# Optimization experiments

Measured on AMD Instinct MI355X. Metric: run time of the kernel, lower is better.

## Reference

```python
import jax, jax.numpy as jnp
import numpy as np

D_MODEL = 1024
N_HEADS = 16
D_FF = 4 * D_MODEL
CTX = 2048
EPS = 1e-5


def setup_inputs() -> dict:
    key = jax.random.key(0)
    ks = jax.random.split(key, 8)
    s = 0.02
    z = jax.random.normal(ks[0], (2, CTX, D_MODEL), dtype=jnp.float32)
    W_Q = jax.random.normal(ks[1], (D_MODEL, D_MODEL), dtype=jnp.float32) * s
    W_K = jax.random.normal(ks[2], (D_MODEL, D_MODEL), dtype=jnp.float32) * s
    W_V = jax.random.normal(ks[3], (D_MODEL, D_MODEL), dtype=jnp.float32) * s
    W_O = jax.random.normal(ks[4], (D_MODEL, D_MODEL), dtype=jnp.float32) * s
    W_fc = jax.random.normal(ks[5], (D_MODEL, D_FF), dtype=jnp.float32) * s
    W_proj = jax.random.normal(ks[6], (D_FF, D_MODEL), dtype=jnp.float32) * s
    g1 = jnp.ones((D_MODEL,), dtype=jnp.float32)
    g2 = jnp.ones((D_MODEL,), dtype=jnp.float32)
    return {"z": z, "W_Q": W_Q, "W_K": W_K, "W_V": W_V, "W_O": W_O,
            "W_fc": W_fc, "W_proj": W_proj, "g1": g1, "g2": g2}


def rmsnorm(x, gain):
    rms = jnp.sqrt(jnp.sum(x * x, axis=-1, keepdims=True) / x.shape[-1] + EPS)
    return (x / rms) * gain


def gelu_erf(x):
    return x * 0.5 * (1.0 + jax.lax.erf(x / jnp.sqrt(2.0).astype(x.dtype)))


def attention(zn, W_Q, W_K, W_V, W_O):
    B, T, D = zn.shape
    H = N_HEADS
    dh = D // H
    # [B,T,D] -> [B,H,T,dh]
    def split(x):
        return x.reshape(B, T, H, dh).transpose(0, 2, 1, 3)
    Q = split(zn @ W_Q)
    K = split(zn @ W_K)
    V = split(zn @ W_V)
    scores = jnp.einsum('bhtd,bhsd->bhts', Q, K) / jnp.sqrt(jnp.float32(dh))
    causal = jnp.triu(jnp.ones((T, T), dtype=bool), k=1)  # True above diagonal -> masked
    scores = jnp.where(causal[None, None], -jnp.inf, scores)
    weights = jax.nn.softmax(scores, axis=-1)
    ctx = jnp.einsum('bhts,bhsd->bhtd', weights, V)
    ctx = ctx.transpose(0, 2, 1, 3).reshape(B, T, D)
    return ctx @ W_O


def reference(z, W_Q, W_K, W_V, W_O, W_fc, W_proj, g1, g2):
    # pre-norm GPT block: z + attn(norm1(z)); then + ffn(norm2(z))
    z = z + attention(rmsnorm(z, g1), W_Q, W_K, W_V, W_O)
    h = rmsnorm(z, g2)
    ffn = gelu_erf(h @ W_fc) @ W_proj
    return z + ffn
```

## Files before the change

### kernel.cpp

```cpp
#include <hip/hip_runtime.h>
#include <hip/hip_bf16.h>
#include <math.h>


typedef __bf16 bf16x8 __attribute__((ext_vector_type(8)));
typedef float  f32x4  __attribute__((ext_vector_type(4)));

#define MFMA_16x16x32_BF16(A, B, C) __builtin_amdgcn_mfma_f32_16x16x32_bf16((A), (B), (C), 0, 0, 0)

#define GLDS16(g, l) __builtin_amdgcn_global_load_lds( \
    (const __attribute__((address_space(1))) void*)(g), \
    (__attribute__((address_space(3))) void*)(l), 16, 0, 0)

__device__ __forceinline__ float fmax3(float a, float b, float c) {
    return fmaxf(fmaxf(a, b), c);
}

__global__ __launch_bounds__(256) void fused_head_kernel(
    const float* __restrict__ W_Q, const float* __restrict__ W_K,
    const float* __restrict__ W_V, const float* __restrict__ W_O,
    const float* __restrict__ W_fc, const float* __restrict__ W_proj,
    __bf16* __restrict__ WtQKV, __bf16* __restrict__ WtO,
    __bf16* __restrict__ Wtfc, __bf16* __restrict__ Wtproj,
    const float* __restrict__ z, const float* __restrict__ g1,
    __bf16* __restrict__ zn)
{
    const int id = blockIdx.x;
    if (id >= 12288) {
        const int row = id - 12288, t = threadIdx.x;
        const float4 v = ((const float4*)(z + (size_t)row * 1024))[t];
        float ss = v.x * v.x + v.y * v.y + v.z * v.z + v.w * v.w;
#pragma unroll
        for (int m = 1; m < 64; m <<= 1) ss += __shfl_xor(ss, m);
        __shared__ float red[4];
        const int wid = t >> 6, lane = t & 63;
        if (lane == 0) red[wid] = ss;
        __syncthreads();
        const float tot = red[0] + red[1] + red[2] + red[3];
        const float inv = rsqrtf(tot * (1.0f / 1024.0f) + 1e-5f);
        const float4 gv = ((const float4*)g1)[t];
        __bf16* o = zn + (size_t)row * 1024 + t * 4;
        o[0] = (__bf16)(v.x * inv * gv.x);
        o[1] = (__bf16)(v.y * inv * gv.y);
        o[2] = (__bf16)(v.z * inv * gv.z);
        o[3] = (__bf16)(v.w * inv * gv.w);
        return;
    }
    const float* src;
    __bf16* dst;
    int K, N, nx, t;
    if (id < 4096) {
        const int wsel = id >> 10;
        t = id & 1023;
        src = (wsel == 0) ? W_Q : (wsel == 1) ? W_K : (wsel == 2) ? W_V : W_O;
        dst = (wsel < 3) ? (WtQKV + (size_t)wsel * 1048576) : WtO;
        K = 1024; N = 1024; nx = 32;
    } else if (id < 8192) {
        t = id - 4096; src = W_fc; dst = Wtfc; K = 1024; N = 4096; nx = 128;
    } else {
        t = id - 8192; src = W_proj; dst = Wtproj; K = 4096; N = 1024; nx = 32;
    }
    const int n0 = (t % nx) * 32, k0 = (t / nx) * 32;

    __shared__ float tile[32][33];
    const int c = threadIdx.x & 31, r = threadIdx.x >> 5;
#pragma unroll
    for (int i = 0; i < 4; ++i)
        tile[r + 8 * i][c] = src[(size_t)(k0 + r + 8 * i) * N + n0 + c];
    __syncthreads();
#pragma unroll
    for (int i = 0; i < 4; ++i)
        dst[(size_t)(n0 + r + 8 * i) * K + k0 + c] = (__bf16)tile[c][r + 8 * i];
}

__global__ __launch_bounds__(256) void rmsnorm_kernel(
    const float* __restrict__ x, const float* __restrict__ gain,
    __bf16* __restrict__ out)
{
    const int row = blockIdx.x, t = threadIdx.x;
    const float4 v = ((const float4*)(x + (size_t)row * 1024))[t];
    float ss = v.x * v.x + v.y * v.y + v.z * v.z + v.w * v.w;
#pragma unroll
    for (int m = 1; m < 64; m <<= 1) ss += __shfl_xor(ss, m);
    __shared__ float red[4];
    const int wid = t >> 6, lane = t & 63;
    if (lane == 0) red[wid] = ss;
    __syncthreads();
    const float tot = red[0] + red[1] + red[2] + red[3];
    const float inv = rsqrtf(tot * (1.0f / 1024.0f) + 1e-5f);
    const float4 gv = ((const float4*)gain)[t];
    __bf16* o = out + (size_t)row * 1024 + t * 4;
    o[0] = (__bf16)(v.x * inv * gv.x);
    o[1] = (__bf16)(v.y * inv * gv.y);
    o[2] = (__bf16)(v.z * inv * gv.z);
    o[3] = (__bf16)(v.w * inv * gv.w);
}

__global__ __launch_bounds__(256) void reduce_add_kernel(
    float* __restrict__ out, const __bf16* __restrict__ p0,
    const __bf16* __restrict__ p1, int n8)
{
    for (int i = blockIdx.x * 256 + threadIdx.x; i < n8; i += gridDim.x * 256) {
        const bf16x8 a = ((const bf16x8*)p0)[i];
        const bf16x8 b = ((const bf16x8*)p1)[i];
        float4 o0 = ((float4*)out)[2 * i];
        float4 o1 = ((float4*)out)[2 * i + 1];
        o0.x += (float)a[0] + (float)b[0]; o0.y += (float)a[1] + (float)b[1];
        o0.z += (float)a[2] + (float)b[2]; o0.w += (float)a[3] + (float)b[3];
        o1.x += (float)a[4] + (float)b[4]; o1.y += (float)a[5] + (float)b[5];
        o1.z += (float)a[6] + (float)b[6]; o1.w += (float)a[7] + (float)b[7];
        ((float4*)out)[2 * i] = o0;
        ((float4*)out)[2 * i + 1] = o1;
    }
}

template <int EPI>
__device__ __forceinline__ void epi_write(
    void* outp, const float* res, int N, int rowg, int colg, float v)
{
    if constexpr (EPI == 1) {
        const size_t idx = (size_t)rowg * N + colg;
        ((float*)outp)[idx] = res[idx] + v;
    } else if constexpr (EPI == 2) {
        const size_t idx = (size_t)rowg * N + colg;
        const float u = v * (1.0f + 0.044715f * v * v) * 2.3022585093f;
        const float r = __builtin_amdgcn_rcpf(1.0f + exp2f(u));
        ((__bf16*)outp)[idx] = (__bf16)(v - v * r);
    }
}

template <int EPI>
__global__ __launch_bounds__(512, 2) void gemm256(
    const __bf16* __restrict__ A, const __bf16* __restrict__ Bt,
    void* __restrict__ outp, const float* __restrict__ res,
    int M, int N, int K)
{
    __shared__ __bf16 As[2][2][128 * 64];
    __shared__ __bf16 Bs[2][2][128 * 64];
    const int tid = threadIdx.x;

    const int gx = gridDim.x, nwg = gx * gridDim.y;
    int bid = blockIdx.y * gx + blockIdx.x;
    int m0, n0;
    if (gx == 16 && gridDim.y == 16) {
        const int xcd = bid & 7, c = bid >> 3;
        const int rm = xcd >> 1, rn = xcd & 1;
        m0 = (rm * 4 + (c >> 3)) * 256;
        n0 = (rn * 8 + (c & 7)) * 256;
    } else {
        if ((nwg & 7) == 0) bid = (bid & 7) * (nwg >> 3) + (bid >> 3);
        m0 = (bid / gx) * 256; n0 = (bid % gx) * 256;
    }

    const int lane = tid & 63, w = tid >> 6;
    const int wr = w >> 2, wc = w & 3;
    const int lr = lane & 15, g = lane >> 4;
    const int srow8 = lane >> 3, schunk = (lane & 7) ^ srow8;
    const int xk = lr & 7;
    const int wch = wc >> 1, bro = (wc & 1) * 64;

    const __bf16* Ab = A + (size_t)m0 * K;
    const __bf16* Bb = Bt + (size_t)n0 * K;

    auto STG = [&](const __bf16* gb, __bf16* lds, int kt, int half) {
        const __bf16* src = gb + (size_t)(half * 128) * K + (kt << 6);
#pragma unroll
        for (int j = 0; j < 2; ++j) {
            const int sidx = j * 8 + w;
            GLDS16(src + (size_t)(sidx * 8 + srow8) * K + schunk * 8, lds + sidx * 512);
        }
    };

    f32x4 acc[8][4] = {};
    bf16x8 af[2][4], bf[2][4];

#define LAF(BUF, QM) do {                                                       \
    _Pragma("unroll") for (int i_ = 0; i_ < 4; ++i_)                            \
    _Pragma("unroll") for (int kk_ = 0; kk_ < 2; ++kk_)                         \
        af[kk_][i_] = *(const bf16x8*)&As[BUF][wr]                              \
            [((QM) * 64 + i_ * 16 + lr) * 64 + (((kk_ * 4 + g) ^ xk) << 3)];    \
    } while (0)

#define LBF(BUF, QN) do {                                                       \
    _Pragma("unroll") for (int i_ = 0; i_ < 2; ++i_)                            \
    _Pragma("unroll") for (int kk_ = 0; kk_ < 2; ++kk_)                         \
        bf[kk_][(QN) * 2 + i_] = *(const bf16x8*)&Bs[BUF][wch]                  \
            [(bro + ((QN) * 2 + i_) * 16 + lr) * 64 + (((kk_ * 4 + g) ^ xk) << 3)]; \
    } while (0)

#define MMQ(QM, QN) do {                                                        \
    __builtin_amdgcn_s_setprio(1);                                              \
    _Pragma("unroll") for (int kk_ = 0; kk_ < 2; ++kk_)                         \
    _Pragma("unroll") for (int i_ = 0; i_ < 4; ++i_)                            \
    _Pragma("unroll") for (int n_ = 0; n_ < 2; ++n_)                            \
        acc[(QM) * 4 + i_][(QN) * 2 + n_] = MFMA_16x16x32_BF16(                 \
            af[kk_][i_], bf[kk_][(QN) * 2 + n_], acc[(QM) * 4 + i_][(QN) * 2 + n_]); \
    __builtin_amdgcn_s_setprio(0);                                              \
    } while (0)

#define BAR()  __builtin_amdgcn_s_barrier()
#define VMC(N_) asm volatile("s_waitcnt vmcnt(" #N_ ")" ::: "memory")
#define SGB0() __builtin_amdgcn_sched_barrier(0)

    const int nt = K >> 6, niter = nt >> 1;

    STG(Ab, &As[0][0][0], 0, 0); STG(Ab, &As[0][1][0], 0, 1);
    STG(Bb, &Bs[0][0][0], 0, 0); STG(Bb, &Bs[0][1][0], 0, 1);
    STG(Bb, &Bs[1][0][0], 1, 0); STG(Bb, &Bs[1][1][0], 1, 1);

    for (int i = 0; i < niter - 1; ++i) {
        const int t1 = 2 * i + 1;
        STG(Ab, &As[1][0][0], t1, 0);
        VMC(6); BAR(); SGB0();
        LAF(0, 0); LBF(0, 0); MMQ(0, 0); BAR();
        LBF(0, 1); STG(Ab, &As[1][1][0], t1, 1); BAR(); MMQ(0, 1); BAR();
        LAF(0, 1); STG(Bb, &Bs[0][0][0], t1 + 1, 0); BAR(); MMQ(1, 0); BAR();
        STG(Bb, &Bs[0][1][0], t1 + 1, 1); BAR(); MMQ(1, 1); BAR();
        STG(Ab, &As[0][0][0], t1 + 1, 0);
        VMC(6); BAR(); SGB0();
        LAF(1, 0); LBF(1, 0); MMQ(0, 0); BAR();
        LBF(1, 1); STG(Ab, &As[0][1][0], t1 + 1, 1); BAR(); MMQ(0, 1); BAR();
        LAF(1, 1); STG(Bb, &Bs[1][0][0], t1 + 2, 0); BAR(); MMQ(1, 0); BAR();
        STG(Bb, &Bs[1][1][0], t1 + 2, 1); BAR(); MMQ(1, 1); BAR();
    }
    {
        STG(Ab, &As[1][0][0], nt - 1, 0);
        VMC(6); BAR(); SGB0();
        LAF(0, 0); LBF(0, 0); MMQ(0, 0); BAR();
        LBF(0, 1); STG(Ab, &As[1][1][0], nt - 1, 1); BAR(); MMQ(0, 1); BAR();
        LAF(0, 1); BAR(); MMQ(1, 0); BAR();
        BAR(); MMQ(1, 1); BAR();
        VMC(0); BAR(); SGB0();
        LAF(1, 0); LBF(1, 0); MMQ(0, 0); BAR();
        LBF(1, 1); BAR(); MMQ(0, 1); BAR();
        LAF(1, 1); BAR(); MMQ(1, 0); BAR();
        BAR(); MMQ(1, 1); BAR();
    }
#undef LAF
#undef LBF
#undef MMQ
#undef BAR
#undef VMC
#undef SGB0

#pragma unroll
    for (int mi = 0; mi < 8; ++mi)
#pragma unroll
        for (int ni = 0; ni < 4; ++ni) {
            const int colg = n0 + wc * 64 + ni * 16 + lr;
#pragma unroll
            for (int r = 0; r < 4; ++r) {
                const int rowg = m0 + wr * 128 + mi * 16 + 4 * g + r;
                epi_write<EPI>(outp, res, N, rowg, colg, acc[mi][ni][r]);
            }
        }
}

template <int BM, int BN, int EPI>
__global__ __launch_bounds__(256) void gemm_bf16(
    const __bf16* __restrict__ A, const __bf16* __restrict__ Bt,
    void* __restrict__ outp, const float* __restrict__ res,
    int M, int N, int K, int Kld)
{
    __shared__ __bf16 As[2][BM * 64];
    __shared__ __bf16 Bs[2][BN * 64];
    const int tid = threadIdx.x;

    const int gx = gridDim.x, nwg = gx * gridDim.y;
    int bid = blockIdx.y * gx + blockIdx.x;
    int m0, n0;
    if constexpr (EPI == 4) {
        const int xcd = bid & 7, c = bid >> 3;
        const int rm = xcd >> 1, rn = xcd & 1;
        m0 = (rm * 8 + (c >> 4)) * BM;
        n0 = (rn * 16 + (c & 15)) * BN;
    } else {
        if ((nwg & 7) == 0) bid = (bid & 7) * (nwg >> 3) + (bid >> 3);
        m0 = (bid / gx) * BM; n0 = (bid % gx) * BN;
    }

    const int lane = tid & 63, w = tid >> 6;
    const int wm = w >> 1, wn = w & 1;
    const int lr = lane & 15, g = lane >> 4;
    const int srow = lane >> 3;
    const int scol = ((lane & 7) ^ srow) * 8;
    const int xr8 = lr & 7;

    constexpr int MI = BM / 32, NI = BN / 32;
    f32x4 acc[MI][NI] = {};

    const __bf16* Abase = A + (size_t)m0 * Kld + blockIdx.z * K;
    const __bf16* Bbase = Bt + (size_t)n0 * Kld + blockIdx.z * K;

    auto STAGE = [&](int kb, int buf) {
#pragma unroll
        for (int j = 0; j < BM / 32; ++j) {
            const int s = j * 4 + w;
            GLDS16(Abase + (size_t)(s * 8 + srow) * Kld + kb + scol, &As[buf][s * 512]);
        }
#pragma unroll
        for (int j = 0; j < BN / 32; ++j) {
            const int s = j * 4 + w;
            GLDS16(Bbase + (size_t)(s * 8 + srow) * Kld + kb + scol, &Bs[buf][s * 512]);
        }
    };

    const int nt = K >> 6;
    STAGE(0, 0);
    __syncthreads();

    for (int t = 0; t < nt; ++t) {
        const int cur = t & 1;
        if (t + 1 < nt) STAGE((t + 1) << 6, cur ^ 1);

        bf16x8 af[2][MI], bfr[2][NI];
#pragma unroll
        for (int kk = 0; kk < 2; ++kk) {
#pragma unroll
            for (int i = 0; i < MI; ++i)
                af[kk][i] = *(const bf16x8*)
                    &As[cur][(wm * (BM / 2) + i * 16 + lr) * 64 + (((kk * 4 + g) ^ xr8) << 3)];
#pragma unroll
            for (int i = 0; i < NI; ++i)
                bfr[kk][i] = *(const bf16x8*)
                    &Bs[cur][(wn * (BN / 2) + i * 16 + lr) * 64 + (((kk * 4 + g) ^ xr8) << 3)];
        }
#pragma unroll
        for (int kk = 0; kk < 2; ++kk)
#pragma unroll
            for (int mi = 0; mi < MI; ++mi)
#pragma unroll
                for (int ni = 0; ni < NI; ++ni)
                    acc[mi][ni] = MFMA_16x16x32_BF16(af[kk][mi], bfr[kk][ni], acc[mi][ni]);
        if (t + 1 < nt) __syncthreads();
    }

    if constexpr (EPI == 4) {
        __bf16* vtile = (__bf16*)As;
        const bool hasV = (n0 + BN > 2048);
        if (hasV) __syncthreads();
#pragma unroll
        for (int mi = 0; mi < MI; ++mi)
#pragma unroll
            for (int ni = 0; ni < NI; ++ni) {
                const int colg = n0 + wn * (BN / 2) + ni * 16 + lr;
#pragma unroll
                for (int r = 0; r < 4; ++r) {
                    const int rowg = m0 + wm * (BM / 2) + mi * 16 + 4 * g + r;
                    const float v = acc[mi][ni][r];
                    if (colg < 2048) {
                        ((__bf16*)outp)[(size_t)(colg >> 10) * 4194304 +
                                        (size_t)rowg * 1024 + (colg & 1023)] = (__bf16)v;
                    } else {
                        const int trow = rowg - m0;
                        const int r32 = trow & 31;
                        const int p = ((r32 & 12) << 1) | ((r32 >> 2) & 4) | (r32 & 3);
                        vtile[(colg - n0) * 128 + (trow & ~31) + p] = (__bf16)v;
                    }
                }
            }
        if (hasV) {
            __syncthreads();
            const int vstart = (2048 > n0) ? (2048 - n0) : 0;
            const int nvec = (BN - vstart) * 16;
            __bf16* base = (__bf16*)outp;
            const size_t vt0 = 8388608 + (size_t)((m0 >> 11) * 16) * 64 * 2048 +
                               (m0 & 2047);
            for (int v = tid; v < nvec; v += 256) {
                const int vc = vstart + (v >> 4);
                const int t8 = (v & 15) << 3;
                const int cg = (n0 + vc) & 1023;
                const size_t idx = vt0 + ((size_t)(cg >> 6) * 64 + (cg & 63)) * 2048 + t8;
                *(bf16x8*)&base[idx] = *(const bf16x8*)&vtile[vc * 128 + t8];
            }
        }
    } else {
#pragma unroll
        for (int mi = 0; mi < MI; ++mi)
#pragma unroll
            for (int ni = 0; ni < NI; ++ni) {
                const int colg = n0 + wn * (BN / 2) + ni * 16 + lr;
#pragma unroll
                for (int r = 0; r < 4; ++r) {
                    const int rowg = m0 + wm * (BM / 2) + mi * 16 + 4 * g + r;
                    const float v = acc[mi][ni][r];
                    if constexpr (EPI == 5) {
                        __bf16* pout = (blockIdx.z == 0) ? (__bf16*)outp
                                                         : (__bf16*)(void*)res;
                        pout[(size_t)rowg * N + colg] = (__bf16)v;
                    } else {
                        epi_write<EPI>(outp, res, N, rowg, colg, v);
                    }
                }
            }
    }
}

__global__ __launch_bounds__(512) void attn_kernel(
    const __bf16* __restrict__ Q, const __bf16* __restrict__ Kb,
    const __bf16* __restrict__ Vt, __bf16* __restrict__ ctx)
{
    const int Dm = 1024, T = 2048;
    const int tid = threadIdx.x;
    const int w = tid >> 6, lane = tid & 63;
    const int lr = lane & 15, g = lane >> 4;
    const int bx = blockIdx.x;
    const int j = bx >> 5, bh = bx & 31, b = bh >> 4, h = bh & 15;
    const int qc = (j < 8) ? j : 23 - j;
    const int qbase = qc * 128 + w * 16;
    const size_t rowoff = (size_t)b * T;
    const __bf16* Qp = Q + rowoff * Dm + h * 64;
    const __bf16* Kp = Kb + rowoff * Dm + h * 64;
    const __bf16* Vtp = Vt + (size_t)bh * 64 * 2048;

    __shared__ __bf16 Ks[2][128 * 64];
    __shared__ __bf16 Vs[2][64 * 128];

    bf16x8 qf0 = *(const bf16x8*)&Qp[(size_t)(qbase + lr) * Dm + g * 8];
    bf16x8 qf1 = *(const bf16x8*)&Qp[(size_t)(qbase + lr) * Dm + 32 + g * 8];
    const float qsc = 0.125f * 1.44269504088896340736f;
#pragma unroll
    for (int jj = 0; jj < 8; ++jj) {
        qf0[jj] = (__bf16)((float)qf0[jj] * qsc);
        qf1[jj] = (__bf16)((float)qf1[jj] * qsc);
    }
    bf16x8 ones;
#pragma unroll
    for (int jj = 0; jj < 8; ++jj) ones[jj] = (__bf16)1.0f;

    const int ksrow = lane >> 3;
    const int kschunk = (lane & 7) ^ ksrow;
    const int vsrow = lane >> 4;

    f32x4 acc[4] = {};
    f32x4 accS = {};
    float m_s = -__builtin_inff();
    const int nsteps = qc + 1;
    const f32x4 zacc = {0.0f, 0.0f, 0.0f, 0.0f};
    const int x8 = lr & 7;
    const int qg = qbase + lr;

    auto STAGE = [&](int kvb, int buf) {
#pragma unroll
        for (int jj = 0; jj < 2; ++jj) {
            const int krow = w * 16 + jj * 8;
            GLDS16(Kp + (size_t)(kvb + krow + ksrow) * Dm + kschunk * 8,
                   &Ks[buf][krow * 64]);
            const int vrow = w * 8 + jj * 4;
            const int vchunk = (lane & 15) ^ ((vrow + vsrow) & 15);
            GLDS16(Vtp + (size_t)(vrow + vsrow) * T + kvb + vchunk * 8,
                   &Vs[buf][vrow * 128]);
        }
    };

    STAGE(0, 0);
    __syncthreads();

    for (int t = 0; t < nsteps; ++t) {
        const int kvb = t * 128, cur = t & 1;
        if (t + 1 < nsteps) STAGE(kvb + 128, cur ^ 1);

        float sv[8][4];
        if (t < qc) {
#pragma unroll
            for (int s4 = 0; s4 < 8; ++s4) {
                const int row = s4 * 16 + lr;
                const bf16x8 kfa = *(const bf16x8*)&Ks[cur][row * 64 + ((g ^ x8) << 3)];
                const bf16x8 kfb = *(const bf16x8*)&Ks[cur][row * 64 + (((4 + g) ^ x8) << 3)];
                f32x4 st = MFMA_16x16x32_BF16(kfa, qf0, zacc);
                st = MFMA_16x16x32_BF16(kfb, qf1, st);
#pragma unroll
                for (int r = 0; r < 4; ++r) sv[s4][r] = st[r];
            }
        } else {
#pragma unroll
            for (int s4 = 0; s4 < 8; ++s4) {
                const int kv0 = kvb + s4 * 16;
                if (kv0 <= qbase + 15) {
                    const int row = s4 * 16 + lr;
                    const bf16x8 kfa = *(const bf16x8*)&Ks[cur][row * 64 + ((g ^ x8) << 3)];
                    const bf16x8 kfb = *(const bf16x8*)&Ks[cur][row * 64 + (((4 + g) ^ x8) << 3)];
                    f32x4 st = MFMA_16x16x32_BF16(kfa, qf0, zacc);
                    st = MFMA_16x16x32_BF16(kfb, qf1, st);
                    const bool domask = (kv0 + 15 > qbase);
#pragma unroll
                    for (int r = 0; r < 4; ++r) {
                        float x = st[r];
                        if (domask && (kv0 + 4 * g + r > qg)) x = -__builtin_inff();
                        sv[s4][r] = x;
                    }
                } else {
#pragma unroll
                    for (int r = 0; r < 4; ++r) sv[s4][r] = -__builtin_inff();
                }
            }
        }

        float tml = fmax3(sv[0][0], sv[0][1], sv[0][2]);
        tml = fmax3(tml, sv[0][3], sv[1][0]);
        tml = fmax3(tml, sv[1][1], sv[1][2]);
        tml = fmax3(tml, sv[1][3], sv[2][0]);
        tml = fmax3(tml, sv[2][1], sv[2][2]);
        tml = fmax3(tml, sv[2][3], sv[3][0]);
        tml = fmax3(tml, sv[3][1], sv[3][2]);
        tml = fmax3(tml, sv[3][3], sv[4][0]);
        tml = fmax3(tml, sv[4][1], sv[4][2]);
        tml = fmax3(tml, sv[4][3], sv[5][0]);
        tml = fmax3(tml, sv[5][1], sv[5][2]);
        tml = fmax3(tml, sv[5][3], sv[6][0]);
        tml = fmax3(tml, sv[6][1], sv[6][2]);
        tml = fmax3(tml, sv[6][3], sv[7][0]);
        tml = fmax3(tml, sv[7][1], sv[7][2]);
        tml = fmaxf(tml, sv[7][3]);

        if (!__all(tml - m_s <= 11.5f)) {
            float tm = fmaxf(tml, __shfl_xor(tml, 16));
            tm = fmaxf(tm, __shfl_xor(tm, 32));
            const float m_new = fmaxf(m_s, tm);
            const float corr = exp2f(m_s - m_new);
            float cr[4];
#pragma unroll
            for (int r = 0; r < 4; ++r) cr[r] = __shfl(corr, 4 * g + r);
#pragma unroll
            for (int ct = 0; ct < 4; ++ct) {
                acc[ct][0] *= cr[0]; acc[ct][1] *= cr[1];
                acc[ct][2] *= cr[2]; acc[ct][3] *= cr[3];
            }
            accS[0] *= cr[0]; accS[1] *= cr[1];
            accS[2] *= cr[2]; accS[3] *= cr[3];
            m_s = m_new;
        }

#pragma unroll
        for (int s4 = 0; s4 < 8; ++s4)
#pragma unroll
            for (int r = 0; r < 4; ++r)
                sv[s4][r] = exp2f(sv[s4][r] - m_s);

        bf16x8 pa[4];
#pragma unroll
        for (int s = 0; s < 4; ++s)
#pragma unroll
            for (int r = 0; r < 4; ++r) {
                pa[s][r] = (__bf16)sv[2 * s][r];
                pa[s][4 + r] = (__bf16)sv[2 * s + 1][r];
            }
        if (t < qc) {
#pragma unroll
            for (int s = 0; s < 4; ++s)
                accS = MFMA_16x16x32_BF16(pa[s], ones, accS);
#pragma unroll
            for (int ct = 0; ct < 4; ++ct) {
                const __bf16* vrow = &Vs[cur][(ct * 16 + lr) * 128];
#pragma unroll
                for (int s = 0; s < 4; ++s) {
                    const bf16x8 vf = *(const bf16x8*)&vrow[(((s * 4 + g) ^ lr) << 3)];
                    acc[ct] = MFMA_16x16x32_BF16(pa[s], vf, acc[ct]);
                }
            }
        } else {
#pragma unroll
            for (int s = 0; s < 4; ++s)
                if (kvb + s * 32 <= qbase + 15)
                    accS = MFMA_16x16x32_BF16(pa[s], ones, accS);
#pragma unroll
            for (int ct = 0; ct < 4; ++ct) {
                const __bf16* vrow = &Vs[cur][(ct * 16 + lr) * 128];
#pragma unroll
                for (int s = 0; s < 4; ++s) {
                    if (kvb + s * 32 <= qbase + 15) {
                        const bf16x8 vf = *(const bf16x8*)&vrow[(((s * 4 + g) ^ lr) << 3)];
                        acc[ct] = MFMA_16x16x32_BF16(pa[s], vf, acc[ct]);
                    }
                }
            }
        }
        __syncthreads();
    }

    float dn[4];
#pragma unroll
    for (int r = 0; r < 4; ++r) dn[r] = __builtin_amdgcn_rcpf(accS[r]);
#pragma unroll
    for (int ct = 0; ct < 4; ++ct)
#pragma unroll
        for (int r = 0; r < 4; ++r)
            ctx[(rowoff + qbase + 4 * g + r) * Dm + h * 64 + ct * 16 + lr] =
                (__bf16)(acc[ct][r] * dn[r]);
}

extern "C" void kernel_launch(void* const* d_in, const int* in_sizes, int n_in,
                              void* d_out, int out_size, void* d_ws, size_t ws_size,
                              hipStream_t stream)
{
    (void)in_sizes; (void)n_in; (void)out_size; (void)ws_size;
    const float* z      = (const float*)d_in[0];
    const float* W_Q    = (const float*)d_in[1];
    const float* W_K    = (const float*)d_in[2];
    const float* W_V    = (const float*)d_in[3];
    const float* W_O    = (const float*)d_in[4];
    const float* W_fc   = (const float*)d_in[5];
    const float* W_proj = (const float*)d_in[6];
    const float* g1     = (const float*)d_in[7];
    const float* g2     = (const float*)d_in[8];
    float* out = (float*)d_out;

    char* ws = (char*)d_ws;
    const size_t MB = (size_t)1 << 20;
    __bf16* WtQKV  = (__bf16*)(ws + 0 * MB);
    __bf16* WtO    = (__bf16*)(ws + 6 * MB);
    __bf16* Wtfc   = (__bf16*)(ws + 8 * MB);
    __bf16* Wtproj = (__bf16*)(ws + 16 * MB);
    __bf16* zn     = (__bf16*)(ws + 24 * MB);
    __bf16* Qb     = (__bf16*)(ws + 32 * MB);
    __bf16* Kbuf   = (__bf16*)(ws + 40 * MB);
    __bf16* Vtb    = (__bf16*)(ws + 48 * MB);
    __bf16* ffn1   = (__bf16*)(ws + 40 * MB);
    __bf16* part0  = (__bf16*)(ws + 0 * MB);
    __bf16* part1  = (__bf16*)(ws + 24 * MB);
    __bf16* ctx    = zn;
    __bf16* hb     = Qb;

    const int Tt = 2048, Dm = 1024, Bb = 2, M = Bb * Tt, DFF = 4096;
    const dim3 blk256(256), blk512(512);

    fused_head_kernel<<<16384, blk256, 0, stream>>>(
        W_Q, W_K, W_V, W_O, W_fc, W_proj, WtQKV, WtO, Wtfc, Wtproj, z, g1, zn);

    gemm_bf16<128, 96, 4><<<dim3(32, 32), blk256, 0, stream>>>(
        zn, WtQKV, Qb, nullptr, M, 3072, Dm, Dm);

    attn_kernel<<<512, blk512, 0, stream>>>(Qb, Kbuf, Vtb, ctx);

    gemm_bf16<128, 64, 1><<<dim3(16, 32), blk256, 0, stream>>>(
        ctx, WtO, out, z, M, Dm, Dm, Dm);

    rmsnorm_kernel<<<M, blk256, 0, stream>>>(out, g2, hb);

    gemm256<2><<<dim3(16, 16), blk512, 0, stream>>>(
        hb, Wtfc, ffn1, nullptr, M, DFF, Dm);

    gemm_bf16<128, 128, 5><<<dim3(8, 32, 2), blk256, 0, stream>>>(
        ffn1, Wtproj, part0, (const float*)part1, M, Dm, DFF / 2, DFF);

    reduce_add_kernel<<<2048, blk256, 0, stream>>>(out, part0, part1, M * Dm / 8);
}
```

Measured before the change: 223.2 us.

## Run FFN down-projection with 256x256 tiles and 4-way split-K

Result: slower. 227.7 us (+2.0%).

```diff
diff --git a/kernel.cpp b/kernel.cpp
--- a/kernel.cpp
+++ b/kernel.cpp
@@ -96,19 +96,26 @@
     o[3] = (__bf16)(v.w * inv * gv.w);
 }
 
-__global__ __launch_bounds__(256) void reduce_add_kernel(
+__global__ __launch_bounds__(256) void reduce_add4_kernel(
     float* __restrict__ out, const __bf16* __restrict__ p0,
-    const __bf16* __restrict__ p1, int n8)
+    const __bf16* __restrict__ p1, const __bf16* __restrict__ p2,
+    const __bf16* __restrict__ p3, int n8)
 {
     for (int i = blockIdx.x * 256 + threadIdx.x; i < n8; i += gridDim.x * 256) {
         const bf16x8 a = ((const bf16x8*)p0)[i];
         const bf16x8 b = ((const bf16x8*)p1)[i];
+        const bf16x8 c = ((const bf16x8*)p2)[i];
+        const bf16x8 d = ((const bf16x8*)p3)[i];
         float4 o0 = ((float4*)out)[2 * i];
         float4 o1 = ((float4*)out)[2 * i + 1];
-        o0.x += (float)a[0] + (float)b[0]; o0.y += (float)a[1] + (float)b[1];
-        o0.z += (float)a[2] + (float)b[2]; o0.w += (float)a[3] + (float)b[3];
-        o1.x += (float)a[4] + (float)b[4]; o1.y += (float)a[5] + (float)b[5];
-        o1.z += (float)a[6] + (float)b[6]; o1.w += (float)a[7] + (float)b[7];
+        o0.x += (float)a[0] + (float)b[0] + (float)c[0] + (float)d[0];
+        o0.y += (float)a[1] + (float)b[1] + (float)c[1] + (float)d[1];
+        o0.z += (float)a[2] + (float)b[2] + (float)c[2] + (float)d[2];
+        o0.w += (float)a[3] + (float)b[3] + (float)c[3] + (float)d[3];
+        o1.x += (float)a[4] + (float)b[4] + (float)c[4] + (float)d[4];
+        o1.y += (float)a[5] + (float)b[5] + (float)c[5] + (float)d[5];
+        o1.z += (float)a[6] + (float)b[6] + (float)c[6] + (float)d[6];
+        o1.w += (float)a[7] + (float)b[7] + (float)c[7] + (float)d[7];
         ((float4*)out)[2 * i] = o0;
         ((float4*)out)[2 * i + 1] = o1;
     }
@@ -129,11 +136,13 @@
     }
 }
 
+__device__ __constant__ size_t POFF[4] = {0, 4194304, 12582912, 16777216};
+
 template <int EPI>
 __global__ __launch_bounds__(512, 2) void gemm256(
     const __bf16* __restrict__ A, const __bf16* __restrict__ Bt,
     void* __restrict__ outp, const float* __restrict__ res,
-    int M, int N, int K)
+    int M, int N, int K, int Kld)
 {
     __shared__ __bf16 As[2][2][128 * 64];
     __shared__ __bf16 Bs[2][2][128 * 64];
@@ -159,15 +168,15 @@
     const int xk = lr & 7;
     const int wch = wc >> 1, bro = (wc & 1) * 64;
 
-    const __bf16* Ab = A + (size_t)m0 * K;
-    const __bf16* Bb = Bt + (size_t)n0 * K;
+    const __bf16* Ab = A + (size_t)m0 * Kld + (size_t)blockIdx.z * K;
+    const __bf16* Bb = Bt + (size_t)n0 * Kld + (size_t)blockIdx.z * K;
 
     auto STG = [&](const __bf16* gb, __bf16* lds, int kt, int half) {
-        const __bf16* src = gb + (size_t)(half * 128) * K + (kt << 6);
+        const __bf16* src = gb + (size_t)(half * 128) * Kld + (kt << 6);
 #pragma unroll
         for (int j = 0; j < 2; ++j) {
             const int sidx = j * 8 + w;
-            GLDS16(src + (size_t)(sidx * 8 + srow8) * K + schunk * 8, lds + sidx * 512);
+            GLDS16(src + (size_t)(sidx * 8 + srow8) * Kld + schunk * 8, lds + sidx * 512);
         }
     };
 
@@ -243,17 +252,32 @@
 #undef VMC
 #undef SGB0
 
-#pragma unroll
-    for (int mi = 0; mi < 8; ++mi)
-#pragma unroll
-        for (int ni = 0; ni < 4; ++ni) {
-            const int colg = n0 + wc * 64 + ni * 16 + lr;
-#pragma unroll
-            for (int r = 0; r < 4; ++r) {
-                const int rowg = m0 + wr * 128 + mi * 16 + 4 * g + r;
-                epi_write<EPI>(outp, res, N, rowg, colg, acc[mi][ni][r]);
-            }
-        }
+    if constexpr (EPI == 5) {
+        __bf16* pout = (__bf16*)outp + POFF[blockIdx.z];
+#pragma unroll
+        for (int mi = 0; mi < 8; ++mi)
+#pragma unroll
+            for (int ni = 0; ni < 4; ++ni) {
+                const int colg = n0 + wc * 64 + ni * 16 + lr;
+#pragma unroll
+                for (int r = 0; r < 4; ++r) {
+                    const int rowg = m0 + wr * 128 + mi * 16 + 4 * g + r;
+                    pout[(size_t)rowg * N + colg] = (__bf16)acc[mi][ni][r];
+                }
+            }
+    } else {
+#pragma unroll
+        for (int mi = 0; mi < 8; ++mi)
+#pragma unroll
+            for (int ni = 0; ni < 4; ++ni) {
+                const int colg = n0 + wc * 64 + ni * 16 + lr;
+#pragma unroll
+                for (int r = 0; r < 4; ++r) {
+                    const int rowg = m0 + wr * 128 + mi * 16 + 4 * g + r;
+                    epi_write<EPI>(outp, res, N, rowg, colg, acc[mi][ni][r]);
+                }
+            }
+    }
 }
 
 template <int BM, int BN, int EPI>
@@ -383,14 +407,7 @@
 #pragma unroll
                 for (int r = 0; r < 4; ++r) {
                     const int rowg = m0 + wm * (BM / 2) + mi * 16 + 4 * g + r;
-                    const float v = acc[mi][ni][r];
-                    if constexpr (EPI == 5) {
-                        __bf16* pout = (blockIdx.z == 0) ? (__bf16*)outp
-                                                         : (__bf16*)(void*)res;
-                        pout[(size_t)rowg * N + colg] = (__bf16)v;
-                    } else {
-                        epi_write<EPI>(outp, res, N, rowg, colg, v);
-                    }
+                    epi_write<EPI>(outp, res, N, rowg, colg, acc[mi][ni][r]);
                 }
             }
     }
@@ -617,7 +634,9 @@
     __bf16* Vtb    = (__bf16*)(ws + 48 * MB);
     __bf16* ffn1   = (__bf16*)(ws + 40 * MB);
     __bf16* part0  = (__bf16*)(ws + 0 * MB);
-    __bf16* part1  = (__bf16*)(ws + 24 * MB);
+    __bf16* part1  = (__bf16*)(ws + 8 * MB);
+    __bf16* part2  = (__bf16*)(ws + 24 * MB);
+    __bf16* part3  = (__bf16*)(ws + 32 * MB);
     __bf16* ctx    = zn;
     __bf16* hb     = Qb;
 
@@ -638,10 +657,11 @@
     rmsnorm_kernel<<<M, blk256, 0, stream>>>(out, g2, hb);
 
     gemm256<2><<<dim3(16, 16), blk512, 0, stream>>>(
-        hb, Wtfc, ffn1, nullptr, M, DFF, Dm);
-
-    gemm_bf16<128, 128, 5><<<dim3(8, 32, 2), blk256, 0, stream>>>(
-        ffn1, Wtproj, part0, (const float*)part1, M, Dm, DFF / 2, DFF);
-
-    reduce_add_kernel<<<2048, blk256, 0, stream>>>(out, part0, part1, M * Dm / 8);
-}
+        hb, Wtfc, ffn1, nullptr, M, DFF, Dm, Dm);
+
+    gemm256<5><<<dim3(4, 16, 4), blk512, 0, stream>>>(
+        ffn1, Wtproj, part0, nullptr, M, Dm, DFF / 4, DFF);
+
+    reduce_add4_kernel<<<2048, blk256, 0, stream>>>(
+        out, part0, part1, part2, part3, M * Dm / 8);
+}
```

## Split causal attention KV range in two and add a combine kernel

Applied to the files above, without the earlier changes.

Result: slower. 232.8 us (+4.3%).

```diff
diff --git a/kernel.cpp b/kernel.cpp
--- a/kernel.cpp
+++ b/kernel.cpp
@@ -398,15 +398,17 @@
 
 __global__ __launch_bounds__(512) void attn_kernel(
     const __bf16* __restrict__ Q, const __bf16* __restrict__ Kb,
-    const __bf16* __restrict__ Vt, __bf16* __restrict__ ctx)
+    const __bf16* __restrict__ Vt, __bf16* __restrict__ Op,
+    float* __restrict__ Sp, float* __restrict__ Mp)
 {
     const int Dm = 1024, T = 2048;
     const int tid = threadIdx.x;
     const int w = tid >> 6, lane = tid & 63;
     const int lr = lane & 15, g = lane >> 4;
     const int bx = blockIdx.x;
-    const int j = bx >> 5, bh = bx & 31, b = bh >> 4, h = bh & 15;
-    const int qc = (j < 8) ? j : 23 - j;
+    const int half = bx & 1, up = bx >> 1;
+    const int j = up >> 5, bh = up & 31, b = bh >> 4, h = bh & 15;
+    const int qc = 15 - j;
     const int qbase = qc * 128 + w * 16;
     const size_t rowoff = (size_t)b * T;
     const __bf16* Qp = Q + rowoff * Dm + h * 64;
@@ -434,8 +436,10 @@
 
     f32x4 acc[4] = {};
     f32x4 accS = {};
-    float m_s = -__builtin_inff();
-    const int nsteps = qc + 1;
+    float m_s = 0.0f;
+    const int h0 = (qc + 2) >> 1;
+    const int t0 = half ? h0 : 0;
+    const int t1 = half ? (qc + 1) : h0;
     const f32x4 zacc = {0.0f, 0.0f, 0.0f, 0.0f};
     const int x8 = lr & 7;
     const int qg = qbase + lr;
@@ -453,12 +457,14 @@
         }
     };
 
-    STAGE(0, 0);
-    __syncthreads();
-
-    for (int t = 0; t < nsteps; ++t) {
+    if (t0 < t1) {
+        STAGE(t0 * 128, t0 & 1);
+        __syncthreads();
+    }
+
+    for (int t = t0; t < t1; ++t) {
         const int kvb = t * 128, cur = t & 1;
-        if (t + 1 < nsteps) STAGE(kvb + 128, cur ^ 1);
+        if (t + 1 < t1) STAGE(kvb + 128, cur ^ 1);
 
         float sv[8][4];
         if (t < qc) {
@@ -578,15 +584,51 @@
         __syncthreads();
     }
 
-    float dn[4];
-#pragma unroll
-    for (int r = 0; r < 4; ++r) dn[r] = __builtin_amdgcn_rcpf(accS[r]);
+    const int hb = ((bh * 16 + qc) << 1) | half;
+    __bf16* Oh = Op + (size_t)hb * 8192;
 #pragma unroll
     for (int ct = 0; ct < 4; ++ct)
 #pragma unroll
         for (int r = 0; r < 4; ++r)
-            ctx[(rowoff + qbase + 4 * g + r) * Dm + h * 64 + ct * 16 + lr] =
-                (__bf16)(acc[ct][r] * dn[r]);
+            Oh[(w * 16 + 4 * g + r) * 64 + ct * 16 + lr] = (__bf16)acc[ct][r];
+    if (lr == 0) {
+#pragma unroll
+        for (int r = 0; r < 4; ++r)
+            Sp[hb * 128 + w * 16 + 4 * g + r] = accS[r];
+    }
+    if (g == 0) {
+        Mp[hb * 128 + w * 16 + lr] = m_s;
+    }
+}
+
+__global__ __launch_bounds__(256) void attn_combine_kernel(
+    const __bf16* __restrict__ Op, const float* __restrict__ Sp,
+    const float* __restrict__ Mp, __bf16* __restrict__ ctx)
+{
+    const int u = blockIdx.x;
+    const int bh = u >> 4, qc = u & 15;
+    const int b = bh >> 4, h = bh & 15;
+    const int row = threadIdx.x >> 1, dh = (threadIdx.x & 1) * 32;
+    const int hb0 = u * 2, hb1 = hb0 + 1;
+    const float mA = Mp[hb0 * 128 + row], mB = Mp[hb1 * 128 + row];
+    const float M = fmaxf(mA, mB);
+    const float eA = exp2f(mA - M), eB = exp2f(mB - M);
+    const float den = Sp[hb0 * 128 + row] * eA + Sp[hb1 * 128 + row] * eB;
+    const float inv = __builtin_amdgcn_rcpf(den);
+    const float fA = eA * inv, fB = eB * inv;
+    const __bf16* OA = Op + (size_t)hb0 * 8192 + row * 64 + dh;
+    const __bf16* OB = Op + (size_t)hb1 * 8192 + row * 64 + dh;
+    __bf16* co = ctx + ((size_t)(b * 2048 + qc * 128 + row)) * 1024 + h * 64 + dh;
+#pragma unroll
+    for (int k = 0; k < 4; ++k) {
+        const bf16x8 a = *(const bf16x8*)&OA[k * 8];
+        const bf16x8 bv = *(const bf16x8*)&OB[k * 8];
+        bf16x8 o;
+#pragma unroll
+        for (int e = 0; e < 8; ++e)
+            o[e] = (__bf16)((float)a[e] * fA + (float)bv[e] * fB);
+        *(bf16x8*)&co[k * 8] = o;
+    }
 }
 
 extern "C" void kernel_launch(void* const* d_in, const int* in_sizes, int n_in,
@@ -615,6 +657,9 @@
     __bf16* Qb     = (__bf16*)(ws + 32 * MB);
     __bf16* Kbuf   = (__bf16*)(ws + 40 * MB);
     __bf16* Vtb    = (__bf16*)(ws + 48 * MB);
+    __bf16* Opart  = (__bf16*)(ws + 56 * MB);
+    float*  Spart  = (float*)(ws + 0 * MB);
+    float*  Mpart  = (float*)(ws + 0 * MB + 524288);
     __bf16* ffn1   = (__bf16*)(ws + 40 * MB);
     __bf16* part0  = (__bf16*)(ws + 0 * MB);
     __bf16* part1  = (__bf16*)(ws + 24 * MB);
@@ -630,7 +675,8 @@
     gemm_bf16<128, 96, 4><<<dim3(32, 32), blk256, 0, stream>>>(
         zn, WtQKV, Qb, nullptr, M, 3072, Dm, Dm);
 
-    attn_kernel<<<512, blk512, 0, stream>>>(Qb, Kbuf, Vtb, ctx);
+    attn_kernel<<<1024, blk512, 0, stream>>>(Qb, Kbuf, Vtb, Opart, Spart, Mpart);
+    attn_combine_kernel<<<512, blk256, 0, stream>>>(Opart, Spart, Mpart, ctx);
 
     gemm_bf16<128, 64, 1><<<dim3(16, 32), blk256, 0, stream>>>(
         ctx, WtO, out, z, M, Dm, Dm, Dm);
```
